# Kernel tuning notes

Hardware: AMD Instinct MI355X
Metric: run time of the kernel (lower is better)

Reference implementation:

```python
import jax, jax.numpy as jnp
import numpy as np

N = 50000      # nodes
E = 800000     # edges (before self-loops)
DIN = 128
DH = 16        # per-head channels, layer 1
H = 8          # heads, layer 1
DOUT = 128     # layer 2 output (heads=1)
EDIM = 8       # edge_attr dim (unused by math: edge_dim=None in GATConv)
EPS_BN = 1e-5
NEG_SLOPE = 0.2


def _gat_conv(x, edge_index, W, a_src, a_dst, bias, heads, ch):
    """PyG GATConv (concat=True, add_self_loops=True, edge_dim=None)."""
    n = x.shape[0]
    loop = jnp.arange(n, dtype=edge_index.dtype)
    src = jnp.concatenate([edge_index[0], loop])  # [E+N]
    dst = jnp.concatenate([edge_index[1], loop])
    h = (x @ W).reshape(n, heads, ch)             # [N,H,C]
    s_src = jnp.einsum('nhc,hc->nh', h, a_src)    # [N,H]
    s_dst = jnp.einsum('nhc,hc->nh', h, a_dst)
    e = jax.nn.leaky_relu(s_src[src] + s_dst[dst], NEG_SLOPE)  # [E+N,H]
    # segment softmax over incoming edges of each dst node
    m = jax.ops.segment_max(e, dst, num_segments=n)
    ex = jnp.exp(e - m[dst])
    den = jax.ops.segment_sum(ex, dst, num_segments=n)
    alpha = ex / (den[dst] + 1e-16)               # [E+N,H]
    out = jax.ops.segment_sum(alpha[:, :, None] * h[src], dst, num_segments=n)
    return out.reshape(n, heads * ch) + bias


def _bn_selu(x, gamma, beta):
    # BatchNorm1d in training mode (batch statistics, biased variance) + SELU.
    mu = x.mean(axis=0)
    var = x.var(axis=0)
    xn = (x - mu) * jax.lax.rsqrt(var + EPS_BN)
    return jax.nn.selu(gamma * xn + beta)


def setup_inputs() -> dict:
    key = jax.random.key(0)
    ks = jax.random.split(key, 12)
    x = jax.random.normal(ks[0], (N, DIN), jnp.float32)
    edge_index = jax.random.randint(ks[1], (2, E), 0, N, jnp.int32)
    edge_attr = jax.random.normal(ks[2], (E, EDIM), jnp.float32)
    W1 = jax.random.normal(ks[3], (DIN, H * DH), jnp.float32) / np.sqrt(DIN)
    a_src1 = jax.random.normal(ks[4], (H, DH), jnp.float32) / np.sqrt(DH)
    a_dst1 = jax.random.normal(ks[5], (H, DH), jnp.float32) / np.sqrt(DH)
    b1 = jnp.zeros((H * DH,), jnp.float32)
    g1 = jnp.ones((H * DH,), jnp.float32)
    beta1 = jnp.zeros((H * DH,), jnp.float32)
    W2 = jax.random.normal(ks[6], (H * DH, DOUT), jnp.float32) / np.sqrt(H * DH)
    a_src2 = jax.random.normal(ks[7], (1, DOUT), jnp.float32) / np.sqrt(DOUT)
    a_dst2 = jax.random.normal(ks[8], (1, DOUT), jnp.float32) / np.sqrt(DOUT)
    b2 = jnp.zeros((DOUT,), jnp.float32)
    g2 = jnp.ones((DOUT,), jnp.float32)
    beta2 = jnp.zeros((DOUT,), jnp.float32)
    return dict(x=x, edge_index=edge_index, edge_attr=edge_attr,
                W1=W1, a_src1=a_src1, a_dst1=a_dst1, b1=b1, g1=g1, beta1=beta1,
                W2=W2, a_src2=a_src2, a_dst2=a_dst2, b2=b2, g2=g2, beta2=beta2)


def reference(x, edge_index, edge_attr,
              W1, a_src1, a_dst1, b1, g1, beta1,
              W2, a_src2, a_dst2, b2, g2, beta2):
    # edge_attr is unused: GATConv built with edge_dim=None ignores edge features.
    h = _gat_conv(x, edge_index, W1, a_src1, a_dst1, b1, H, DH)   # [N, H*DH]
    h = _bn_selu(h, g1, beta1)                                    # dropout = identity (eval)
    h = _gat_conv(h, edge_index, W2, a_src2, a_dst2, b2, 1, DOUT) # [N, DOUT]
    h = _bn_selu(h, g2, beta2)
    return h
```

## Files before the change

### kernel.cpp

```cpp
#include <hip/hip_runtime.h>

#define SELU_SCALE 1.0507009873554805f
#define SELU_ALPHA 1.6732632423543772f

typedef __attribute__((ext_vector_type(8))) short short8;
typedef __attribute__((ext_vector_type(4))) float f32x4;

#define BCAP 20480

static __device__ __forceinline__ float leaky02(float v) {
  return v > 0.0f ? v : 0.2f * v;
}

static __device__ __forceinline__ ushort f2bf(float f) {
  uint b = __float_as_uint(f);
  return (ushort)((b + 0x7fffu + ((b >> 16) & 1u)) >> 16);
}
static __device__ __forceinline__ float bf2f(ushort u) {
  return __uint_as_float(((uint)u) << 16);
}

static __device__ __forceinline__ float selu_f(float y) {
  return y > 0.f ? SELU_SCALE * y : SELU_SCALE * SELU_ALPHA * (__expf(y) - 1.f);
}

__global__ __launch_bounds__(256) void pack_kernel(const float* __restrict__ W1,
                                                   const float* __restrict__ W2,
                                                   ushort* __restrict__ Wp1,
                                                   ushort* __restrict__ Wp2) {
  int idx = blockIdx.x * 256 + threadIdx.x;
  const float* W = (idx < 16384) ? W1 : W2;
  ushort* Wp = (idx < 16384) ? Wp1 : Wp2;
  int t = idx & 16383;
  int b = t & 7, i = (t >> 3) & 15, g = (t >> 7) & 3, kt = (t >> 9) & 3, ct = t >> 11;
  int k = kt * 32 + g * 8 + b, col = ct * 16 + i;
  Wp[t] = f2bf(W[k * 128 + col]);
}

template <int HEADS, bool BN>
static __device__ __forceinline__ void gemm_body(
    int blk, const float* __restrict__ X, const ushort* __restrict__ Wp,
    ushort* __restrict__ H, const float* __restrict__ asr, const float* __restrict__ adt,
    float* __restrict__ ssrc, float* __restrict__ sdst, int n,
    const float* __restrict__ stats, const float* __restrict__ gamma,
    const float* __restrict__ beta) {
  __shared__ float sc[128], sh[128];
  if (BN) {
    int t = threadIdx.x;
    if (t < 128) {
      float invN = 1.0f / (float)n;
      float mu = stats[t] * invN;
      float var = stats[128 + t] * invN - mu * mu;
      float rs = rsqrtf(var + 1e-5f);
      float s = gamma[t] * rs;
      sc[t] = s;
      sh[t] = beta[t] - s * mu;
    }
    __syncthreads();
  }
  const int tid = threadIdx.x;
  const int w = tid >> 6, l = tid & 63;
  const int lj = l & 15, lg = l >> 4;
  const int row = blk * 64 + w * 16 + lj;
  const bool rowok = row < n;
  const float* xrow = X + (size_t)row * 128;

  f32x4 acc[8];
#pragma unroll
  for (int ct = 0; ct < 8; ++ct) acc[ct] = (f32x4){0.f, 0.f, 0.f, 0.f};

#pragma unroll
  for (int kt = 0; kt < 4; ++kt) {
    const int k0 = kt * 32 + lg * 8;
    float4 xa = make_float4(0.f, 0.f, 0.f, 0.f), xb = xa;
    if (rowok) {
      xa = *(const float4*)(xrow + k0);
      xb = *(const float4*)(xrow + k0 + 4);
    }
    float xv[8] = {xa.x, xa.y, xa.z, xa.w, xb.x, xb.y, xb.z, xb.w};
    if (BN) {
#pragma unroll
      for (int b = 0; b < 8; ++b) xv[b] = selu_f(xv[b] * sc[k0 + b] + sh[k0 + b]);
    }
    short8 bx;
#pragma unroll
    for (int b = 0; b < 8; ++b) bx[b] = (short)f2bf(xv[b]);
#pragma unroll
    for (int ct = 0; ct < 8; ++ct) {
      short8 af = *(const short8*)(Wp + ((((ct * 4 + kt) * 4 + lg) * 16 + lj) << 3));
      acc[ct] = __builtin_amdgcn_mfma_f32_16x16x32_bf16(af, bx, acc[ct], 0, 0, 0);
    }
  }

  if (rowok) {
#pragma unroll
    for (int ct = 0; ct < 8; ++ct) {
      ushort4 h4;
      h4.x = f2bf(acc[ct][0]);
      h4.y = f2bf(acc[ct][1]);
      h4.z = f2bf(acc[ct][2]);
      h4.w = f2bf(acc[ct][3]);
      *(ushort4*)&H[(size_t)row * 128 + ct * 16 + lg * 4] = h4;
    }
  }

  if (HEADS == 8) {
    float ps[8], pd[8];
#pragma unroll
    for (int ct = 0; ct < 8; ++ct) {
      float4 av = *(const float4*)&asr[ct * 16 + lg * 4];
      float4 dv = *(const float4*)&adt[ct * 16 + lg * 4];
      ps[ct] = acc[ct][0] * av.x + acc[ct][1] * av.y + acc[ct][2] * av.z + acc[ct][3] * av.w;
      pd[ct] = acc[ct][0] * dv.x + acc[ct][1] * dv.y + acc[ct][2] * dv.z + acc[ct][3] * dv.w;
      ps[ct] += __shfl_xor(ps[ct], 16);
      ps[ct] += __shfl_xor(ps[ct], 32);
      pd[ct] += __shfl_xor(pd[ct], 16);
      pd[ct] += __shfl_xor(pd[ct], 32);
    }
    if (lg == 0 && rowok) {
      *(float4*)&ssrc[(size_t)row * 8] = make_float4(ps[0], ps[1], ps[2], ps[3]);
      *(float4*)&ssrc[(size_t)row * 8 + 4] = make_float4(ps[4], ps[5], ps[6], ps[7]);
      *(float4*)&sdst[(size_t)row * 8] = make_float4(pd[0], pd[1], pd[2], pd[3]);
      *(float4*)&sdst[(size_t)row * 8 + 4] = make_float4(pd[4], pd[5], pd[6], pd[7]);
    }
  } else {
    float ps = 0.f, pd = 0.f;
#pragma unroll
    for (int ct = 0; ct < 8; ++ct) {
      float4 av = *(const float4*)&asr[ct * 16 + lg * 4];
      float4 dv = *(const float4*)&adt[ct * 16 + lg * 4];
      ps += acc[ct][0] * av.x + acc[ct][1] * av.y + acc[ct][2] * av.z + acc[ct][3] * av.w;
      pd += acc[ct][0] * dv.x + acc[ct][1] * dv.y + acc[ct][2] * dv.z + acc[ct][3] * dv.w;
    }
    ps += __shfl_xor(ps, 16);
    ps += __shfl_xor(ps, 32);
    pd += __shfl_xor(pd, 16);
    pd += __shfl_xor(pd, 32);
    if (lg == 0 && rowok) {
      ssrc[row] = ps;
      sdst[row] = pd;
    }
  }
}

__global__ __launch_bounds__(256) void gemm1_bucket_kernel(
    const float* __restrict__ X, const ushort* __restrict__ Wp, ushort* __restrict__ H,
    const float* __restrict__ asr, const float* __restrict__ adt,
    float* __restrict__ ssrc, float* __restrict__ sdst, int n,
    const int* __restrict__ ei, int* __restrict__ gcur, uint* __restrict__ bucket,
    int nE, int EA, int NB, int gb) {
  if (blockIdx.x < gb) {
    gemm_body<8, false>(blockIdx.x, X, Wp, H, asr, adt, ssrc, sdst, n,
                        nullptr, nullptr, nullptr);
    return;
  }
  __shared__ int lcnt[64];
  __shared__ int lbase[64];
  int tid = threadIdx.x;
  if (tid < 64) lcnt[tid] = 0;
  __syncthreads();
  int e0 = (blockIdx.x - gb) * 1024;
  uint ent[4];
  int bk[4], lp[4];
#pragma unroll
  for (int j = 0; j < 4; ++j) {
    int e = e0 + j * 256 + tid;
    bk[j] = -1;
    if (e < EA) {
      int src, dst;
      if (e < nE) {
        src = ei[e];
        dst = ei[nE + e];
      } else {
        src = dst = e - nE;
      }
      bk[j] = dst >> 10;
      ent[j] = ((uint)src << 10) | (uint)(dst & 1023);
      lp[j] = atomicAdd(&lcnt[bk[j]], 1);
    }
  }
  __syncthreads();
  if (tid < NB && lcnt[tid] > 0) lbase[tid] = atomicAdd(&gcur[tid], lcnt[tid]);
  __syncthreads();
#pragma unroll
  for (int j = 0; j < 4; ++j) {
    if (bk[j] >= 0) bucket[(size_t)bk[j] * BCAP + lbase[bk[j]] + lp[j]] = ent[j];
  }
}

template <int HEADS, bool BN>
__global__ __launch_bounds__(256) void gemm_mfma_kernel(
    const float* __restrict__ X, const ushort* __restrict__ Wp, ushort* __restrict__ H,
    const float* __restrict__ asr, const float* __restrict__ adt,
    float* __restrict__ ssrc, float* __restrict__ sdst, int n,
    const float* __restrict__ stats, const float* __restrict__ gamma,
    const float* __restrict__ beta) {
  gemm_body<HEADS, BN>(blockIdx.x, X, Wp, H, asr, adt, ssrc, sdst, n, stats, gamma, beta);
}

__global__ __launch_bounds__(1024) void csrbuild_kernel(const int* __restrict__ gcur,
                                                        const uint* __restrict__ bucket,
                                                        int* __restrict__ offs,
                                                        int* __restrict__ csr,
                                                        int n, int NB) {
  __shared__ int ldeg[1024];
  __shared__ int loff[1024];
  __shared__ int lwsum[16];
  __shared__ int sbase;
  int b = blockIdx.x, tid = threadIdx.x;
  int lane = tid & 63, w = tid >> 6;
  if (tid < 64) {
    int v = (tid < NB) ? gcur[tid] : 0;
    int x = v;
#pragma unroll
    for (int s = 1; s < 64; s <<= 1) {
      int t = __shfl_up(x, s);
      if (tid >= s) x += t;
    }
    if (tid == b) sbase = x - v;
  }
  ldeg[tid] = 0;
  __syncthreads();
  int base = sbase;
  int cnt = gcur[b];
  const uint* bb = bucket + (size_t)b * BCAP;
  for (int k = tid; k < cnt; k += 1024) atomicAdd(&ldeg[bb[k] & 1023], 1);
  __syncthreads();
  int v = ldeg[tid];
  int x = v;
#pragma unroll
  for (int s = 1; s < 64; s <<= 1) {
    int t = __shfl_up(x, s);
    if (lane >= s) x += t;
  }
  if (lane == 63) lwsum[w] = x;
  __syncthreads();
  if (w == 0 && lane < 16) {
    int wv = lwsum[lane];
    int y = wv;
#pragma unroll
    for (int s = 1; s < 16; s <<= 1) {
      int t = __shfl_up(y, s);
      if (lane >= s) y += t;
    }
    lwsum[lane] = y - wv;
  }
  __syncthreads();
  int excl = x - v + lwsum[w];
  loff[tid] = excl;
  int node = b * 1024 + tid;
  if (node < n) offs[node] = base + excl;
  if (b == NB - 1 && tid == 0) offs[n] = base + cnt;
  __syncthreads();
  ldeg[tid] = loff[tid];
  __syncthreads();
  for (int k = tid; k < cnt; k += 1024) {
    uint e = bb[k];
    int pos = atomicAdd(&ldeg[e & 1023], 1);
    csr[base + pos] = (int)(e >> 10);
  }
}

__global__ __launch_bounds__(256) void agg1_kernel(const ushort* __restrict__ h1,
                                                   const int* __restrict__ csr,
                                                   const int* __restrict__ offs,
                                                   const float* __restrict__ ssrc,
                                                   const float* __restrict__ sdst,
                                                   const float* __restrict__ bias,
                                                   float* __restrict__ out, int nN) {
  int wid = (blockIdx.x * blockDim.x + threadIdx.x) >> 6;
  int lane = threadIdx.x & 63;
  int half = lane >> 5, ll = lane & 31;
  if (wid >= nN) return;
  int c = ll * 4;
  int h = ll >> 2;
  float sd = sdst[wid * 8 + h];
  int beg = offs[wid];
  int deg = offs[wid + 1] - beg;
  float a0 = 0.f, a1 = 0.f, a2 = 0.f, a3 = 0.f, den = 0.f;
  int i = half;
  for (; i + 6 < deg; i += 8) {
    int s0 = csr[beg + i];
    int s1 = csr[beg + i + 2];
    int s2 = csr[beg + i + 4];
    int s3 = csr[beg + i + 6];
    float e0 = ssrc[s0 * 8 + h];
    float e1 = ssrc[s1 * 8 + h];
    float e2 = ssrc[s2 * 8 + h];
    float e3 = ssrc[s3 * 8 + h];
    ushort4 u0 = *(const ushort4*)&h1[(size_t)s0 * 128 + c];
    ushort4 u1 = *(const ushort4*)&h1[(size_t)s1 * 128 + c];
    ushort4 u2 = *(const ushort4*)&h1[(size_t)s2 * 128 + c];
    ushort4 u3 = *(const ushort4*)&h1[(size_t)s3 * 128 + c];
    float A0 = __expf(leaky02(e0 + sd));
    float A1 = __expf(leaky02(e1 + sd));
    float A2 = __expf(leaky02(e2 + sd));
    float A3 = __expf(leaky02(e3 + sd));
    a0 += A0 * bf2f(u0.x) + A1 * bf2f(u1.x) + A2 * bf2f(u2.x) + A3 * bf2f(u3.x);
    a1 += A0 * bf2f(u0.y) + A1 * bf2f(u1.y) + A2 * bf2f(u2.y) + A3 * bf2f(u3.y);
    a2 += A0 * bf2f(u0.z) + A1 * bf2f(u1.z) + A2 * bf2f(u2.z) + A3 * bf2f(u3.z);
    a3 += A0 * bf2f(u0.w) + A1 * bf2f(u1.w) + A2 * bf2f(u2.w) + A3 * bf2f(u3.w);
    den += (A0 + A1) + (A2 + A3);
  }
  for (; i < deg; i += 2) {
    int s0 = csr[beg + i];
    float e0 = ssrc[s0 * 8 + h];
    ushort4 u0 = *(const ushort4*)&h1[(size_t)s0 * 128 + c];
    float A0 = __expf(leaky02(e0 + sd));
    a0 += A0 * bf2f(u0.x);
    a1 += A0 * bf2f(u0.y);
    a2 += A0 * bf2f(u0.z);
    a3 += A0 * bf2f(u0.w);
    den += A0;
  }
  a0 += __shfl_xor(a0, 32);
  a1 += __shfl_xor(a1, 32);
  a2 += __shfl_xor(a2, 32);
  a3 += __shfl_xor(a3, 32);
  den += __shfl_xor(den, 32);
  if (half == 0) {
    float invd = 1.0f / (den + 1e-16f);
    float4 bv = *(const float4*)&bias[c];
    *(float4*)&out[(size_t)wid * 128 + c] =
        make_float4(a0 * invd + bv.x, a1 * invd + bv.y, a2 * invd + bv.z, a3 * invd + bv.w);
  }
}

__global__ __launch_bounds__(256) void agg2_kernel(const ushort* __restrict__ h2,
                                                   const int* __restrict__ csr,
                                                   const int* __restrict__ offs,
                                                   const float* __restrict__ ssrc,
                                                   const float* __restrict__ sdst,
                                                   const float* __restrict__ bias,
                                                   float* __restrict__ out, int nN) {
  int wid = (blockIdx.x * blockDim.x + threadIdx.x) >> 6;
  int lane = threadIdx.x & 63;
  int half = lane >> 5, ll = lane & 31;
  if (wid >= nN) return;
  int c = ll * 4;
  float sd = sdst[wid];
  int beg = offs[wid];
  int deg = offs[wid + 1] - beg;
  float a0 = 0.f, a1 = 0.f, a2 = 0.f, a3 = 0.f, den = 0.f;
  int i = half;
  for (; i + 6 < deg; i += 8) {
    int s0 = csr[beg + i];
    int s1 = csr[beg + i + 2];
    int s2 = csr[beg + i + 4];
    int s3 = csr[beg + i + 6];
    float e0 = ssrc[s0];
    float e1 = ssrc[s1];
    float e2 = ssrc[s2];
    float e3 = ssrc[s3];
    ushort4 u0 = *(const ushort4*)&h2[(size_t)s0 * 128 + c];
    ushort4 u1 = *(const ushort4*)&h2[(size_t)s1 * 128 + c];
    ushort4 u2 = *(const ushort4*)&h2[(size_t)s2 * 128 + c];
    ushort4 u3 = *(const ushort4*)&h2[(size_t)s3 * 128 + c];
    float A0 = __expf(leaky02(e0 + sd));
    float A1 = __expf(leaky02(e1 + sd));
    float A2 = __expf(leaky02(e2 + sd));
    float A3 = __expf(leaky02(e3 + sd));
    a0 += A0 * bf2f(u0.x) + A1 * bf2f(u1.x) + A2 * bf2f(u2.x) + A3 * bf2f(u3.x);
    a1 += A0 * bf2f(u0.y) + A1 * bf2f(u1.y) + A2 * bf2f(u2.y) + A3 * bf2f(u3.y);
    a2 += A0 * bf2f(u0.z) + A1 * bf2f(u1.z) + A2 * bf2f(u2.z) + A3 * bf2f(u3.z);
    a3 += A0 * bf2f(u0.w) + A1 * bf2f(u1.w) + A2 * bf2f(u2.w) + A3 * bf2f(u3.w);
    den += (A0 + A1) + (A2 + A3);
  }
  for (; i < deg; i += 2) {
    int s0 = csr[beg + i];
    float e0 = ssrc[s0];
    ushort4 u0 = *(const ushort4*)&h2[(size_t)s0 * 128 + c];
    float A0 = __expf(leaky02(e0 + sd));
    a0 += A0 * bf2f(u0.x);
    a1 += A0 * bf2f(u0.y);
    a2 += A0 * bf2f(u0.z);
    a3 += A0 * bf2f(u0.w);
    den += A0;
  }
  a0 += __shfl_xor(a0, 32);
  a1 += __shfl_xor(a1, 32);
  a2 += __shfl_xor(a2, 32);
  a3 += __shfl_xor(a3, 32);
  den += __shfl_xor(den, 32);
  if (half == 0) {
    float invd = 1.0f / (den + 1e-16f);
    float4 bv = *(const float4*)&bias[c];
    *(float4*)&out[(size_t)wid * 128 + c] =
        make_float4(a0 * invd + bv.x, a1 * invd + bv.y, a2 * invd + bv.z, a3 * invd + bv.w);
  }
}

__global__ __launch_bounds__(256) void stats_kernel(const float* __restrict__ X,
                                                    float* __restrict__ stats, int n) {
  __shared__ float red[256];
  int tid = threadIdx.x;
  int c = tid & 127;
  int half = tid >> 7;
  float s = 0.f, sq = 0.f;
  int rbeg = (int)blockIdx.x * 64 + half;
  int rend = min((int)(blockIdx.x + 1) * 64, n);
#pragma unroll 4
  for (int r = rbeg; r < rend; r += 2) {
    float v = X[(size_t)r * 128 + c];
    s += v;
    sq += v * v;
  }
  red[tid] = s;
  __syncthreads();
  float s2 = (half == 0) ? s + red[tid + 128] : 0.f;
  __syncthreads();
  red[tid] = sq;
  __syncthreads();
  if (half == 0) {
    float sq2 = sq + red[tid + 128];
    atomicAdd(&stats[c], s2);
    atomicAdd(&stats[128 + c], sq2);
  }
}

__global__ __launch_bounds__(256) void bnselu_kernel(const float* __restrict__ X,
                                                     const float* __restrict__ stats,
                                                     const float* __restrict__ gamma,
                                                     const float* __restrict__ beta,
                                                     float* __restrict__ Y, int n) {
  int gid = blockIdx.x * blockDim.x + threadIdx.x;
  if (gid >= n * 32) return;
  int c = (gid & 31) * 4;
  int r = gid >> 5;
  float invN = 1.0f / (float)n;
  float4 x = *(const float4*)&X[(size_t)r * 128 + c];
  float o[4];
#pragma unroll
  for (int j = 0; j < 4; ++j) {
    float xx = (j == 0) ? x.x : (j == 1) ? x.y : (j == 2) ? x.z : x.w;
    float mu = stats[c + j] * invN;
    float var = stats[128 + c + j] * invN - mu * mu;
    float rs = rsqrtf(var + 1e-5f);
    float y = gamma[c + j] * ((xx - mu) * rs) + beta[c + j];
    o[j] = selu_f(y);
  }
  *(float4*)&Y[(size_t)r * 128 + c] = make_float4(o[0], o[1], o[2], o[3]);
}

extern "C" void kernel_launch(void* const* d_in, const int* in_sizes, int n_in,
                              void* d_out, int out_size, void* d_ws, size_t ws_size,
                              hipStream_t stream) {
  const float* x   = (const float*)d_in[0];
  const int*   ei  = (const int*)d_in[1];
  const float* W1  = (const float*)d_in[3];
  const float* as1 = (const float*)d_in[4];
  const float* ad1 = (const float*)d_in[5];
  const float* b1  = (const float*)d_in[6];
  const float* g1  = (const float*)d_in[7];
  const float* be1 = (const float*)d_in[8];
  const float* W2  = (const float*)d_in[9];
  const float* as2 = (const float*)d_in[10];
  const float* ad2 = (const float*)d_in[11];
  const float* b2  = (const float*)d_in[12];
  const float* g2  = (const float*)d_in[13];
  const float* be2 = (const float*)d_in[14];
  float* out = (float*)d_out;

  const int n  = in_sizes[0] / 128;
  const int nE = in_sizes[1] / 2;
  const int EA = nE + n;
  const int NB = (n + 1023) >> 10;
  const int nbb = (EA + 1023) / 1024;
  const int gb = (n + 63) / 64;

  float* ws = (float*)d_ws;
  size_t o = 0;
  float* Bf = ws + o;     o += (size_t)n * 128;
  ushort* H = (ushort*)(ws + o); o += (size_t)n * 64;
  float* ssrc1 = ws + o;  o += (size_t)n * 8;
  float* sdst1 = ws + o;  o += (size_t)n * 8;
  float* ssrc2 = ws + o;  o += n;
  float* sdst2 = ws + o;  o += n;
  ushort* Wp1 = (ushort*)(ws + o); o += 8192;
  ushort* Wp2 = (ushort*)(ws + o); o += 8192;
  float* zbase = ws + o;
  float* stats1 = ws + o; o += 256;
  float* stats2 = ws + o; o += 256;
  int* gcur = (int*)(ws + o); o += 64;
  size_t zwords = (size_t)((ws + o) - zbase);
  int* offs = (int*)(ws + o); o += (size_t)n + 1;
  int* csr  = (int*)(ws + o); o += EA;
  uint* bucket = (uint*)(ws + o); o += (size_t)NB * BCAP;

  hipMemsetAsync(zbase, 0, zwords * sizeof(float), stream);

  pack_kernel<<<128, 256, 0, stream>>>(W1, W2, Wp1, Wp2);

  gemm1_bucket_kernel<<<gb + nbb, 256, 0, stream>>>(
      x, Wp1, H, as1, ad1, ssrc1, sdst1, n, ei, gcur, bucket, nE, EA, NB, gb);
  csrbuild_kernel<<<NB, 1024, 0, stream>>>(gcur, bucket, offs, csr, n, NB);

  agg1_kernel<<<(n + 3) / 4, 256, 0, stream>>>(H, csr, offs, ssrc1, sdst1, b1, Bf, n);
  stats_kernel<<<(n + 63) / 64, 256, 0, stream>>>(Bf, stats1, n);

  gemm_mfma_kernel<1, true><<<(n + 63) / 64, 256, 0, stream>>>(
      Bf, Wp2, H, as2, ad2, ssrc2, sdst2, n, stats1, g1, be1);
  agg2_kernel<<<(n + 3) / 4, 256, 0, stream>>>(H, csr, offs, ssrc2, sdst2, b2, out, n);
  stats_kernel<<<(n + 63) / 64, 256, 0, stream>>>(out, stats2, n);
  bnselu_kernel<<<(n * 32 + 255) / 256, 256, 0, stream>>>(out, stats2, g2, be2, out, n);
}
```

Before: 227.3 us.

## Store layer-1 output in bf16, shrink CSR buckets, fold memset into pack

Layer-1 aggregation now writes its output as bf16 instead of fp32. The BN statistics kernel and the layer-2 GEMM read that bf16 buffer, which halves the traffic for this intermediate. CSR bucketing now uses 512-node buckets, giving 98 blocks instead of 49, so the build has more parallelism and each block computes its base with a reduction rather than a scan. The workspace memset moves into an extra block of the pack kernel, removing one API call. The trade-off is that BN statistics are computed from bf16-rounded values, and the bucket capacity assumptions change.

```diff
diff --git a/kernel.cpp b/kernel.cpp
--- a/kernel.cpp
+++ b/kernel.cpp
@@ -6,7 +6,7 @@
 typedef __attribute__((ext_vector_type(8))) short short8;
 typedef __attribute__((ext_vector_type(4))) float f32x4;
 
-#define BCAP 20480
+#define BCAP 10240
 
 static __device__ __forceinline__ float leaky02(float v) {
   return v > 0.0f ? v : 0.2f * v;
@@ -24,10 +24,34 @@
   return y > 0.f ? SELU_SCALE * y : SELU_SCALE * SELU_ALPHA * (__expf(y) - 1.f);
 }
 
+static __device__ __forceinline__ void load8(const float* p, float* xv, bool ok) {
+  float4 xa = make_float4(0.f, 0.f, 0.f, 0.f), xb = xa;
+  if (ok) {
+    xa = *(const float4*)p;
+    xb = *(const float4*)(p + 4);
+  }
+  xv[0] = xa.x; xv[1] = xa.y; xv[2] = xa.z; xv[3] = xa.w;
+  xv[4] = xb.x; xv[5] = xb.y; xv[6] = xb.z; xv[7] = xb.w;
+}
+static __device__ __forceinline__ void load8(const ushort* p, float* xv, bool ok) {
+  ushort4 ua = make_ushort4(0, 0, 0, 0), ub = ua;
+  if (ok) {
+    ua = *(const ushort4*)p;
+    ub = *(const ushort4*)(p + 4);
+  }
+  xv[0] = bf2f(ua.x); xv[1] = bf2f(ua.y); xv[2] = bf2f(ua.z); xv[3] = bf2f(ua.w);
+  xv[4] = bf2f(ub.x); xv[5] = bf2f(ub.y); xv[6] = bf2f(ub.z); xv[7] = bf2f(ub.w);
+}
+
 __global__ __launch_bounds__(256) void pack_kernel(const float* __restrict__ W1,
                                                    const float* __restrict__ W2,
                                                    ushort* __restrict__ Wp1,
-                                                   ushort* __restrict__ Wp2) {
+                                                   ushort* __restrict__ Wp2,
+                                                   float* __restrict__ zbase, int zwords) {
+  if (blockIdx.x == 128) {
+    for (int i = threadIdx.x; i < zwords; i += 256) zbase[i] = 0.f;
+    return;
+  }
   int idx = blockIdx.x * 256 + threadIdx.x;
   const float* W = (idx < 16384) ? W1 : W2;
   ushort* Wp = (idx < 16384) ? Wp1 : Wp2;
@@ -37,9 +61,9 @@
   Wp[t] = f2bf(W[k * 128 + col]);
 }
 
-template <int HEADS, bool BN>
+template <int HEADS, bool BN, typename XT>
 static __device__ __forceinline__ void gemm_body(
-    int blk, const float* __restrict__ X, const ushort* __restrict__ Wp,
+    int blk, const XT* __restrict__ X, const ushort* __restrict__ Wp,
     ushort* __restrict__ H, const float* __restrict__ asr, const float* __restrict__ adt,
     float* __restrict__ ssrc, float* __restrict__ sdst, int n,
     const float* __restrict__ stats, const float* __restrict__ gamma,
@@ -63,7 +87,7 @@
   const int lj = l & 15, lg = l >> 4;
   const int row = blk * 64 + w * 16 + lj;
   const bool rowok = row < n;
-  const float* xrow = X + (size_t)row * 128;
+  const XT* xrow = X + (size_t)row * 128;
 
   f32x4 acc[8];
 #pragma unroll
@@ -72,12 +96,8 @@
 #pragma unroll
   for (int kt = 0; kt < 4; ++kt) {
     const int k0 = kt * 32 + lg * 8;
-    float4 xa = make_float4(0.f, 0.f, 0.f, 0.f), xb = xa;
-    if (rowok) {
-      xa = *(const float4*)(xrow + k0);
-      xb = *(const float4*)(xrow + k0 + 4);
-    }
-    float xv[8] = {xa.x, xa.y, xa.z, xa.w, xb.x, xb.y, xb.z, xb.w};
+    float xv[8];
+    load8(xrow + k0, xv, rowok);
     if (BN) {
 #pragma unroll
       for (int b = 0; b < 8; ++b) xv[b] = selu_f(xv[b] * sc[k0 + b] + sh[k0 + b]);
@@ -150,14 +170,14 @@
     const int* __restrict__ ei, int* __restrict__ gcur, uint* __restrict__ bucket,
     int nE, int EA, int NB, int gb) {
   if (blockIdx.x < gb) {
-    gemm_body<8, false>(blockIdx.x, X, Wp, H, asr, adt, ssrc, sdst, n,
-                        nullptr, nullptr, nullptr);
+    gemm_body<8, false, float>(blockIdx.x, X, Wp, H, asr, adt, ssrc, sdst, n,
+                               nullptr, nullptr, nullptr);
     return;
   }
-  __shared__ int lcnt[64];
-  __shared__ int lbase[64];
+  __shared__ int lcnt[128];
+  __shared__ int lbase[128];
   int tid = threadIdx.x;
-  if (tid < 64) lcnt[tid] = 0;
+  if (tid < 128) lcnt[tid] = 0;
   __syncthreads();
   int e0 = (blockIdx.x - gb) * 1024;
   uint ent[4];
@@ -174,8 +194,8 @@
       } else {
         src = dst = e - nE;
       }
-      bk[j] = dst >> 10;
-      ent[j] = ((uint)src << 10) | (uint)(dst & 1023);
+      bk[j] = dst >> 9;
+      ent[j] = ((uint)src << 9) | (uint)(dst & 511);
       lp[j] = atomicAdd(&lcnt[bk[j]], 1);
     }
   }
@@ -188,14 +208,14 @@
   }
 }
 
-template <int HEADS, bool BN>
-__global__ __launch_bounds__(256) void gemm_mfma_kernel(
-    const float* __restrict__ X, const ushort* __restrict__ Wp, ushort* __restrict__ H,
+__global__ __launch_bounds__(256) void gemm2_kernel(
+    const ushort* __restrict__ X, const ushort* __restrict__ Wp, ushort* __restrict__ H,
     const float* __restrict__ asr, const float* __restrict__ adt,
     float* __restrict__ ssrc, float* __restrict__ sdst, int n,
     const float* __restrict__ stats, const float* __restrict__ gamma,
     const float* __restrict__ beta) {
-  gemm_body<HEADS, BN>(blockIdx.x, X, Wp, H, asr, adt, ssrc, sdst, n, stats, gamma, beta);
+  gemm_body<1, true, ushort>(blockIdx.x, X, Wp, H, asr, adt, ssrc, sdst, n,
+                             stats, gamma, beta);
 }
 
 __global__ __launch_bounds__(1024) void csrbuild_kernel(const int* __restrict__ gcur,
@@ -203,61 +223,62 @@
                                                         int* __restrict__ offs,
                                                         int* __restrict__ csr,
                                                         int n, int NB) {
-  __shared__ int ldeg[1024];
-  __shared__ int loff[1024];
-  __shared__ int lwsum[16];
-  __shared__ int sbase;
+  __shared__ int ldeg[512];
+  __shared__ int loff[512];
+  __shared__ int lwsum[8];
+  __shared__ int partial[2];
   int b = blockIdx.x, tid = threadIdx.x;
   int lane = tid & 63, w = tid >> 6;
-  if (tid < 64) {
-    int v = (tid < NB) ? gcur[tid] : 0;
-    int x = v;
+  if (tid < 128) {
+    int v = (tid < b) ? gcur[tid] : 0;
+#pragma unroll
+    for (int s = 1; s < 64; s <<= 1) v += __shfl_xor(v, s);
+    if (lane == 0) partial[tid >> 6] = v;
+  }
+  if (tid < 512) ldeg[tid] = 0;
+  __syncthreads();
+  int base = partial[0] + partial[1];
+  int cnt = gcur[b];
+  const uint* bb = bucket + (size_t)b * BCAP;
+  for (int k = tid; k < cnt; k += 1024) atomicAdd(&ldeg[bb[k] & 511], 1);
+  __syncthreads();
+  int v = 0, x = 0;
+  if (tid < 512) {
+    v = ldeg[tid];
+    x = v;
 #pragma unroll
     for (int s = 1; s < 64; s <<= 1) {
       int t = __shfl_up(x, s);
-      if (tid >= s) x += t;
-    }
-    if (tid == b) sbase = x - v;
-  }
-  ldeg[tid] = 0;
-  __syncthreads();
-  int base = sbase;
-  int cnt = gcur[b];
-  const uint* bb = bucket + (size_t)b * BCAP;
-  for (int k = tid; k < cnt; k += 1024) atomicAdd(&ldeg[bb[k] & 1023], 1);
-  __syncthreads();
-  int v = ldeg[tid];
-  int x = v;
-#pragma unroll
-  for (int s = 1; s < 64; s <<= 1) {
-    int t = __shfl_up(x, s);
-    if (lane >= s) x += t;
-  }
-  if (lane == 63) lwsum[w] = x;
-  __syncthreads();
-  if (w == 0 && lane < 16) {
+      if (lane >= s) x += t;
+    }
+    if (lane == 63) lwsum[w] = x;
+  }
+  __syncthreads();
+  if (w == 0 && lane < 8) {
     int wv = lwsum[lane];
     int y = wv;
 #pragma unroll
-    for (int s = 1; s < 16; s <<= 1) {
+    for (int s = 1; s < 8; s <<= 1) {
       int t = __shfl_up(y, s);
       if (lane >= s) y += t;
     }
     lwsum[lane] = y - wv;
   }
   __syncthreads();
-  int excl = x - v + lwsum[w];
-  loff[tid] = excl;
-  int node = b * 1024 + tid;
-  if (node < n) offs[node] = base + excl;
+  if (tid < 512) {
+    int excl = x - v + lwsum[w];
+    loff[tid] = excl;
+    int node = b * 512 + tid;
+    if (node < n) offs[node] = base + excl;
+  }
   if (b == NB - 1 && tid == 0) offs[n] = base + cnt;
   __syncthreads();
-  ldeg[tid] = loff[tid];
+  if (tid < 512) ldeg[tid] = loff[tid];
   __syncthreads();
   for (int k = tid; k < cnt; k += 1024) {
     uint e = bb[k];
-    int pos = atomicAdd(&ldeg[e & 1023], 1);
-    csr[base + pos] = (int)(e >> 10);
+    int pos = atomicAdd(&ldeg[e & 511], 1);
+    csr[base + pos] = (int)(e >> 9);
   }
 }
 
@@ -267,7 +288,7 @@
                                                    const float* __restrict__ ssrc,
                                                    const float* __restrict__ sdst,
                                                    const float* __restrict__ bias,
-                                                   float* __restrict__ out, int nN) {
+                                                   ushort* __restrict__ outb, int nN) {
   int wid = (blockIdx.x * blockDim.x + threadIdx.x) >> 6;
   int lane = threadIdx.x & 63;
   int half = lane >> 5, ll = lane & 31;
@@ -321,8 +342,12 @@
   if (half == 0) {
     float invd = 1.0f / (den + 1e-16f);
     float4 bv = *(const float4*)&bias[c];
-    *(float4*)&out[(size_t)wid * 128 + c] =
-        make_float4(a0 * invd + bv.x, a1 * invd + bv.y, a2 * invd + bv.z, a3 * invd + bv.w);
+    ushort4 o;
+    o.x = f2bf(a0 * invd + bv.x);
+    o.y = f2bf(a1 * invd + bv.y);
+    o.z = f2bf(a2 * invd + bv.z);
+    o.w = f2bf(a3 * invd + bv.w);
+    *(ushort4*)&outb[(size_t)wid * 128 + c] = o;
   }
 }
 
@@ -390,6 +415,34 @@
   }
 }
 
+__global__ __launch_bounds__(256) void stats_bf16_kernel(const ushort* __restrict__ X,
+                                                         float* __restrict__ stats, int n) {
+  __shared__ float red[256];
+  int tid = threadIdx.x;
+  int c = tid & 127;
+  int half = tid >> 7;
+  float s = 0.f, sq = 0.f;
+  int rbeg = (int)blockIdx.x * 64 + half;
+  int rend = min((int)(blockIdx.x + 1) * 64, n);
+#pragma unroll 4
+  for (int r = rbeg; r < rend; r += 2) {
+    float v = bf2f(X[(size_t)r * 128 + c]);
+    s += v;
+    sq += v * v;
+  }
+  red[tid] = s;
+  __syncthreads();
+  float s2 = (half == 0) ? s + red[tid + 128] : 0.f;
+  __syncthreads();
+  red[tid] = sq;
+  __syncthreads();
+  if (half == 0) {
+    float sq2 = sq + red[tid + 128];
+    atomicAdd(&stats[c], s2);
+    atomicAdd(&stats[128 + c], sq2);
+  }
+}
+
 __global__ __launch_bounds__(256) void stats_kernel(const float* __restrict__ X,
                                                     float* __restrict__ stats, int n) {
   __shared__ float red[256];
@@ -464,13 +517,13 @@
   const int n  = in_sizes[0] / 128;
   const int nE = in_sizes[1] / 2;
   const int EA = nE + n;
-  const int NB = (n + 1023) >> 10;
+  const int NB = (n + 511) >> 9;
   const int nbb = (EA + 1023) / 1024;
   const int gb = (n + 63) / 64;
 
   float* ws = (float*)d_ws;
   size_t o = 0;
-  float* Bf = ws + o;     o += (size_t)n * 128;
+  ushort* Bf = (ushort*)(ws + o); o += (size_t)n * 64;
   ushort* H = (ushort*)(ws + o); o += (size_t)n * 64;
   float* ssrc1 = ws + o;  o += (size_t)n * 8;
   float* sdst1 = ws + o;  o += (size_t)n * 8;
@@ -481,24 +534,22 @@
   float* zbase = ws + o;
   float* stats1 = ws + o; o += 256;
   float* stats2 = ws + o; o += 256;
-  int* gcur = (int*)(ws + o); o += 64;
-  size_t zwords = (size_t)((ws + o) - zbase);
+  int* gcur = (int*)(ws + o); o += 128;
+  int zwords = (int)((ws + o) - zbase);
   int* offs = (int*)(ws + o); o += (size_t)n + 1;
   int* csr  = (int*)(ws + o); o += EA;
   uint* bucket = (uint*)(ws + o); o += (size_t)NB * BCAP;
 
-  hipMemsetAsync(zbase, 0, zwords * sizeof(float), stream);
-
-  pack_kernel<<<128, 256, 0, stream>>>(W1, W2, Wp1, Wp2);
+  pack_kernel<<<129, 256, 0, stream>>>(W1, W2, Wp1, Wp2, zbase, zwords);
 
   gemm1_bucket_kernel<<<gb + nbb, 256, 0, stream>>>(
       x, Wp1, H, as1, ad1, ssrc1, sdst1, n, ei, gcur, bucket, nE, EA, NB, gb);
   csrbuild_kernel<<<NB, 1024, 0, stream>>>(gcur, bucket, offs, csr, n, NB);
 
   agg1_kernel<<<(n + 3) / 4, 256, 0, stream>>>(H, csr, offs, ssrc1, sdst1, b1, Bf, n);
-  stats_kernel<<<(n + 63) / 64, 256, 0, stream>>>(Bf, stats1, n);
-
-  gemm_mfma_kernel<1, true><<<(n + 63) / 64, 256, 0, stream>>>(
+  stats_bf16_kernel<<<(n + 63) / 64, 256, 0, stream>>>(Bf, stats1, n);
+
+  gemm2_kernel<<<(n + 63) / 64, 256, 0, stream>>>(
       Bf, Wp2, H, as2, ad2, ssrc2, sdst2, n, stats1, g1, be1);
   agg2_kernel<<<(n + 3) / 4, 256, 0, stream>>>(H, csr, offs, ssrc2, sdst2, b2, out, n);
   stats_kernel<<<(n + 63) / 64, 256, 0, stream>>>(out, stats2, n);
```

Result: faster. 222.2 us (median of 2 runs) (-2.3%).
